# Optimization experiments

Measured on AMD Instinct MI355X. Metric: run time of the kernel, lower is better.

The kernel has to match this reference:

```python
import jax, jax.numpy as jnp
import numpy as np

WS = 32          # window_size -> N = WS*WS = 1024
DIM = 1024
HEADS = 16
BATCH = 16


def _local_mask():
    # token i maps to grid cell (i//WS, i%WS); attend iff within 3x3 neighborhood
    idx = jnp.arange(WS * WS)
    r, c = idx // WS, idx % WS
    return (jnp.abs(r[:, None] - r[None, :]) <= 1) & (jnp.abs(c[:, None] - c[None, :]) <= 1)


def setup_inputs() -> dict:
    key = jax.random.key(0)
    k1, k2, k3 = jax.random.split(key, 3)
    N = WS * WS
    x = jax.random.normal(k1, (BATCH, N, DIM), dtype=jnp.float32)
    w_qkv = jax.random.normal(k2, (3 * DIM, DIM), dtype=jnp.float32) * 0.02
    w_proj = jax.random.normal(k3, (DIM, DIM), dtype=jnp.float32) * 0.02
    b_proj = jnp.zeros((DIM,), dtype=jnp.float32)
    return {"x": x, "w_qkv": w_qkv, "w_proj": w_proj, "b_proj": b_proj}


def reference(x, w_qkv, w_proj, b_proj):
    B, N, C = x.shape
    H = HEADS
    D = C // H
    scale = D ** (-0.5)
    # qkv projection: torch Linear is x @ W^T
    qkv = (x @ w_qkv.T).reshape(B, N, 3, H, D).transpose(2, 0, 3, 1, 4)  # (3,B,H,N,D)
    q, k, v = qkv[0], qkv[1], qkv[2]
    attn = jnp.einsum('bhnd,bhmd->bhnm', q, k) * scale  # (B,H,N,N)
    mask = _local_mask()  # (N,N) bool
    attn = jnp.where(mask[None, None], attn, -jnp.inf)
    attn = jax.nn.softmax(attn, axis=-1)
    out = jnp.einsum('bhnm,bhmd->bhnd', attn, v)          # (B,H,N,D)
    out = out.transpose(0, 2, 1, 3).reshape(B, N, C)      # (B,N,C)
    return out @ w_proj.T + b_proj
```

## Files before the change

kernel.cpp:

```cpp
#include <hip/hip_runtime.h>
#include <hip/hip_bf16.h>
#include <stdint.h>


typedef __bf16 bf16;
typedef __bf16 bf16x4_t __attribute__((ext_vector_type(4)));
typedef __bf16 bf16x8_t __attribute__((ext_vector_type(8)));
typedef float f32x4_t __attribute__((ext_vector_type(4)));

static __device__ __forceinline__ void gload_lds16(const void* g, void* l) {
  __builtin_amdgcn_global_load_lds((__attribute__((address_space(1))) void*)g,
                                   (__attribute__((address_space(3))) void*)l,
                                   16, 0, 0);
}

static __device__ __forceinline__ void block_barrier() {
  asm volatile("" ::: "memory");
  __builtin_amdgcn_s_barrier();
  asm volatile("" ::: "memory");
}

__global__ void cvt_f32_bf16(const float* __restrict__ in, bf16* __restrict__ out, int n4) {
  int i = blockIdx.x * blockDim.x + threadIdx.x;
  if (i >= n4) return;
  float4 v = reinterpret_cast<const float4*>(in)[i];
  bf16x4_t o;
  o[0] = (bf16)v.x; o[1] = (bf16)v.y; o[2] = (bf16)v.z; o[3] = (bf16)v.w;
  reinterpret_cast<bf16x4_t*>(out)[i] = o;
}

template<int OUT_BF16>
__global__ __launch_bounds__(512, 2)
void gemm256(const bf16* __restrict__ A, const bf16* __restrict__ Bm,
             void* __restrict__ Cout, const float* __restrict__ bias,
             int M, int N, int K) {
  extern __shared__ __align__(16) bf16 lds[];

  const int tid = threadIdx.x;
  const int w = tid >> 6, lane = tid & 63;
  const int fr = lane & 15, g = lane >> 4;
  const int wr = w >> 2, wc = w & 3;

  const int nwg = gridDim.x * gridDim.y;
  int lid = blockIdx.y * gridDim.x + blockIdx.x;
  lid = (lid & 7) * (nwg >> 3) + (lid >> 3);
  const int bx = lid % gridDim.x, by = lid / gridDim.x;
  const int row0 = by * 256, col0 = bx * 256;

  const bf16* Ag = A + (size_t)row0 * K;
  const bf16* Bg = Bm + (size_t)col0 * K;
  const int rsub = tid >> 3;
  const int csw  = ((tid & 7) * 8) ^ ((rsub & 7) << 3);
  const int nkt  = K >> 6;

  f32x4_t acc[8][4] = {};

  auto stage = [&](int kt, int slot) {
    const int kb = kt << 6;
    bf16* sl = lds + slot * 32768;
#pragma unroll
    for (int n = 0; n < 4; ++n) {
      gload_lds16(Ag + (size_t)(rsub + n * 64) * K + kb + csw,
                  sl + n * 4096 + w * 512);
      gload_lds16(Bg + (size_t)(rsub + n * 64) * K + kb + csw,
                  sl + 16384 + n * 4096 + w * 512);
    }
  };

  const int axor = (fr & 7) << 4;

  stage(0, 0);
  stage(1, 1);
  asm volatile("s_waitcnt vmcnt(8)" ::: "memory");
  block_barrier();

  for (int kt = 0; kt < nkt; ++kt) {
    const char* cA = reinterpret_cast<const char*>(lds + (kt & 1) * 32768);
    const char* cB = cA + 32768;

    bf16x8_t a0[4][2], a1[4][2], b0[2][2], b1[2][2];

    auto lda = [&](bf16x8_t (&dst)[4][2], int q) {
#pragma unroll
      for (int i = 0; i < 4; ++i) {
        const int row = wr * 128 + (q * 4 + i) * 16 + fr;
#pragma unroll
        for (int kh = 0; kh < 2; ++kh) {
          const int bo = (row << 7) + (((kh << 6) + (g << 4)) ^ axor);
          dst[i][kh] = *reinterpret_cast<const bf16x8_t*>(cA + bo);
        }
      }
    };
    auto ldb = [&](bf16x8_t (&dst)[2][2], int q) {
#pragma unroll
      for (int j = 0; j < 2; ++j) {
        const int row = wc * 64 + (q * 2 + j) * 16 + fr;
#pragma unroll
        for (int kh = 0; kh < 2; ++kh) {
          const int bo = (row << 7) + (((kh << 6) + (g << 4)) ^ axor);
          dst[j][kh] = *reinterpret_cast<const bf16x8_t*>(cB + bo);
        }
      }
    };

    lda(a0, 0);
    ldb(b0, 0);
#pragma unroll
    for (int i = 0; i < 4; ++i)
#pragma unroll
      for (int j = 0; j < 2; ++j)
#pragma unroll
        for (int kh = 0; kh < 2; ++kh)
          acc[i][j] = __builtin_amdgcn_mfma_f32_16x16x32_bf16(
              a0[i][kh], b0[j][kh], acc[i][j], 0, 0, 0);
    ldb(b1, 1);
#pragma unroll
    for (int i = 0; i < 4; ++i)
#pragma unroll
      for (int j = 0; j < 2; ++j)
#pragma unroll
        for (int kh = 0; kh < 2; ++kh)
          acc[i][2 + j] = __builtin_amdgcn_mfma_f32_16x16x32_bf16(
              a0[i][kh], b1[j][kh], acc[i][2 + j], 0, 0, 0);
    lda(a1, 1);
#pragma unroll
    for (int i = 0; i < 4; ++i)
#pragma unroll
      for (int j = 0; j < 2; ++j)
#pragma unroll
        for (int kh = 0; kh < 2; ++kh)
          acc[4 + i][2 + j] = __builtin_amdgcn_mfma_f32_16x16x32_bf16(
              a1[i][kh], b1[j][kh], acc[4 + i][2 + j], 0, 0, 0);
#pragma unroll
    for (int i = 0; i < 4; ++i)
#pragma unroll
      for (int j = 0; j < 2; ++j)
#pragma unroll
        for (int kh = 0; kh < 2; ++kh)
          acc[4 + i][j] = __builtin_amdgcn_mfma_f32_16x16x32_bf16(
              a1[i][kh], b0[j][kh], acc[4 + i][j], 0, 0, 0);

    block_barrier();
    if (kt + 2 < nkt) stage(kt + 2, kt & 1);
    if (kt < nkt - 2) {
      asm volatile("s_waitcnt vmcnt(8)" ::: "memory");
    } else {
      asm volatile("s_waitcnt vmcnt(0)" ::: "memory");
    }
    block_barrier();
  }

#pragma unroll
  for (int fm = 0; fm < 8; ++fm) {
    const int rbase = row0 + wr * 128 + fm * 16 + g * 4;
#pragma unroll
    for (int fn = 0; fn < 4; ++fn) {
      const int col = col0 + wc * 64 + fn * 16 + fr;
#pragma unroll
      for (int r = 0; r < 4; ++r) {
        const size_t idx = (size_t)(rbase + r) * N + col;
        if constexpr (OUT_BF16) {
          reinterpret_cast<bf16*>(Cout)[idx] = (bf16)acc[fm][fn][r];
        } else {
          reinterpret_cast<float*>(Cout)[idx] = acc[fm][fn][r] + bias[col];
        }
      }
    }
  }
}

__global__ __launch_bounds__(256)
void local_attn(const bf16* __restrict__ qkv, bf16* __restrict__ outp) {
  const int tid  = threadIdx.x;
  const int wave = tid >> 6, lane = tid & 63;
  const int tsub = lane >> 3, ch = lane & 7;
  const int gt = (blockIdx.x * 4 + wave) * 8 + tsub;
  const int i  = gt & 1023;
  const int bh = gt >> 10;
  const int h  = bh & 15, b = bh >> 4;
  const int r  = i >> 5, c = i & 31;

  const bf16* base = qkv + (size_t)(b * 1024) * 3072 + h * 64 + ch * 8;

  bf16x8_t qv = *reinterpret_cast<const bf16x8_t*>(base + (size_t)i * 3072);
  float qf[8];
#pragma unroll
  for (int e = 0; e < 8; ++e) qf[e] = (float)qv[e];

  float s[9];
  bool valid[9];
#pragma unroll
  for (int dr = -1; dr <= 1; ++dr) {
#pragma unroll
    for (int dc = -1; dc <= 1; ++dc) {
      const int idx = (dr + 1) * 3 + (dc + 1);
      const int rr = r + dr, cc = c + dc;
      valid[idx] = (rr >= 0 && rr < 32 && cc >= 0 && cc < 32);
      float sv = -1e30f;
      if (valid[idx]) {
        const int j = rr * 32 + cc;
        bf16x8_t kv = *reinterpret_cast<const bf16x8_t*>(base + (size_t)j * 3072 + 1024);
        float ps = 0.f;
#pragma unroll
        for (int e = 0; e < 8; ++e) ps += qf[e] * (float)kv[e];
        ps += __shfl_xor(ps, 1);
        ps += __shfl_xor(ps, 2);
        ps += __shfl_xor(ps, 4);
        sv = ps * 0.125f;
      }
      s[idx] = sv;
    }
  }

  float mx = s[0];
#pragma unroll
  for (int t = 1; t < 9; ++t) mx = fmaxf(mx, s[t]);

  float p[9], denom = 0.f;
#pragma unroll
  for (int t = 0; t < 9; ++t) {
    p[t] = valid[t] ? __expf(s[t] - mx) : 0.f;
    denom += p[t];
  }

  float o[8] = {};
#pragma unroll
  for (int dr = -1; dr <= 1; ++dr) {
#pragma unroll
    for (int dc = -1; dc <= 1; ++dc) {
      const int idx = (dr + 1) * 3 + (dc + 1);
      if (valid[idx]) {
        const int j = (r + dr) * 32 + (c + dc);
        bf16x8_t vv = *reinterpret_cast<const bf16x8_t*>(base + (size_t)j * 3072 + 2048);
        const float pw = p[idx];
#pragma unroll
        for (int e = 0; e < 8; ++e) o[e] += pw * (float)vv[e];
      }
    }
  }

  const float inv = 1.f / denom;
  bf16x8_t ov;
#pragma unroll
  for (int e = 0; e < 8; ++e) ov[e] = (bf16)(o[e] * inv);
  *reinterpret_cast<bf16x8_t*>(outp + (size_t)(b * 1024 + i) * 1024 + h * 64 + ch * 8) = ov;
}

extern "C" void kernel_launch(void* const* d_in, const int* in_sizes, int n_in,
                              void* d_out, int out_size, void* d_ws, size_t ws_size,
                              hipStream_t stream) {
  const float* x      = (const float*)d_in[0];
  const float* w_qkv  = (const float*)d_in[1];
  const float* w_proj = (const float*)d_in[2];
  const float* b_proj = (const float*)d_in[3];
  float* out = (float*)d_out;

  const size_t nx   = (size_t)16384 * 1024;
  const size_t nwq  = (size_t)3072 * 1024;
  const size_t nwp  = (size_t)1024 * 1024;
  const size_t nqkv = (size_t)16384 * 3072;

  bf16* x_bf  = (bf16*)d_ws;
  bf16* wq_bf = x_bf + nx;
  bf16* wp_bf = wq_bf + nwq;
  bf16* qkv   = wp_bf + nwp;
  bf16* attn  = qkv + nqkv;

  (void)hipFuncSetAttribute((const void*)&gemm256<1>,
                            hipFuncAttributeMaxDynamicSharedMemorySize, 131072);
  (void)hipFuncSetAttribute((const void*)&gemm256<0>,
                            hipFuncAttributeMaxDynamicSharedMemorySize, 131072);

  cvt_f32_bf16<<<(int)(nx  / 4 / 256), 256, 0, stream>>>(x,      x_bf,  (int)(nx  / 4));
  cvt_f32_bf16<<<(int)(nwq / 4 / 256), 256, 0, stream>>>(w_qkv,  wq_bf, (int)(nwq / 4));
  cvt_f32_bf16<<<(int)(nwp / 4 / 256), 256, 0, stream>>>(w_proj, wp_bf, (int)(nwp / 4));

  gemm256<1><<<dim3(3072 / 256, 16384 / 256), 512, 131072, stream>>>(
      x_bf, wq_bf, qkv, nullptr, 16384, 3072, 1024);

  local_attn<<<8192, 256, 0, stream>>>(qkv, attn);

  gemm256<0><<<dim3(1024 / 256, 16384 / 256), 512, 131072, stream>>>(
      attn, wp_bf, out, b_proj, 16384, 1024, 1024);
}
```

Baseline: 216.1 us.

## Interleave GEMM prefetch with MFMA clusters and merge conversion kernels

The GEMM main loop is split into four MFMA clusters separated by block barriers and raised wave priority (s_setprio). The next tile's B and A global-to-LDS loads are now issued between clusters instead of after all compute, as soon as the corresponding LDS reads have drained. This aims to overlap memory traffic with matrix math and to coordinate the waves on each CU. The three fp32-to-bf16 conversion launches are also merged into one kernel to cut launch overhead. The extra barriers per iteration add synchronisation cost and could stall waves if the schedule does not line up.

```diff
diff --git a/kernel.cpp b/kernel.cpp
--- a/kernel.cpp
+++ b/kernel.cpp
@@ -20,13 +20,19 @@
   asm volatile("" ::: "memory");
 }
 
-__global__ void cvt_f32_bf16(const float* __restrict__ in, bf16* __restrict__ out, int n4) {
+__global__ void cvt_all(const float* __restrict__ x, const float* __restrict__ wq,
+                        const float* __restrict__ wp, bf16* __restrict__ xb,
+                        bf16* __restrict__ wqb, bf16* __restrict__ wpb) {
+  constexpr int NX = 4194304, NWQ = 786432;
   int i = blockIdx.x * blockDim.x + threadIdx.x;
-  if (i >= n4) return;
-  float4 v = reinterpret_cast<const float4*>(in)[i];
+  const float* src; bf16* dst; int off;
+  if (i < NX)            { src = x;  dst = xb;  off = i; }
+  else if (i < NX + NWQ) { src = wq; dst = wqb; off = i - NX; }
+  else                   { src = wp; dst = wpb; off = i - (NX + NWQ); }
+  float4 v = reinterpret_cast<const float4*>(src)[off];
   bf16x4_t o;
   o[0] = (bf16)v.x; o[1] = (bf16)v.y; o[2] = (bf16)v.z; o[3] = (bf16)v.w;
-  reinterpret_cast<bf16x4_t*>(out)[i] = o;
+  reinterpret_cast<bf16x4_t*>(dst)[off] = o;
 }
 
 template<int OUT_BF16>
@@ -55,28 +61,34 @@
 
   f32x4_t acc[8][4] = {};
 
-  auto stage = [&](int kt, int slot) {
+  auto stageA = [&](int kt, int slot) {
     const int kb = kt << 6;
     bf16* sl = lds + slot * 32768;
 #pragma unroll
-    for (int n = 0; n < 4; ++n) {
+    for (int n = 0; n < 4; ++n)
       gload_lds16(Ag + (size_t)(rsub + n * 64) * K + kb + csw,
                   sl + n * 4096 + w * 512);
+  };
+  auto stageB = [&](int kt, int slot) {
+    const int kb = kt << 6;
+    bf16* sl = lds + slot * 32768 + 16384;
+#pragma unroll
+    for (int n = 0; n < 4; ++n)
       gload_lds16(Bg + (size_t)(rsub + n * 64) * K + kb + csw,
-                  sl + 16384 + n * 4096 + w * 512);
-    }
+                  sl + n * 4096 + w * 512);
   };
 
   const int axor = (fr & 7) << 4;
 
-  stage(0, 0);
-  stage(1, 1);
+  stageB(0, 0); stageA(0, 0);
+  stageB(1, 1); stageA(1, 1);
   asm volatile("s_waitcnt vmcnt(8)" ::: "memory");
   block_barrier();
 
   for (int kt = 0; kt < nkt; ++kt) {
     const char* cA = reinterpret_cast<const char*>(lds + (kt & 1) * 32768);
     const char* cB = cA + 32768;
+    const bool pf = (kt + 2 < nkt);
 
     bf16x8_t a0[4][2], a1[4][2], b0[2][2], b1[2][2];
 
@@ -102,47 +114,47 @@
         }
       }
     };
-
-    lda(a0, 0);
-    ldb(b0, 0);
-#pragma unroll
-    for (int i = 0; i < 4; ++i)
-#pragma unroll
-      for (int j = 0; j < 2; ++j)
-#pragma unroll
-        for (int kh = 0; kh < 2; ++kh)
-          acc[i][j] = __builtin_amdgcn_mfma_f32_16x16x32_bf16(
-              a0[i][kh], b0[j][kh], acc[i][j], 0, 0, 0);
+    auto mfma16 = [&](bf16x8_t (&af)[4][2], bf16x8_t (&bf_)[2][2], int mi0, int nj0) {
+      __builtin_amdgcn_s_setprio(1);
+#pragma unroll
+      for (int i = 0; i < 4; ++i)
+#pragma unroll
+        for (int j = 0; j < 2; ++j)
+#pragma unroll
+          for (int kh = 0; kh < 2; ++kh)
+            acc[mi0 + i][nj0 + j] = __builtin_amdgcn_mfma_f32_16x16x32_bf16(
+                af[i][kh], bf_[j][kh], acc[mi0 + i][nj0 + j], 0, 0, 0);
+      __builtin_amdgcn_s_setprio(0);
+    };
+
+    lda(a0, 0); ldb(b0, 0);
+    asm volatile("s_waitcnt lgkmcnt(8)" ::: "memory");
+    block_barrier();
+    asm volatile("s_waitcnt lgkmcnt(0)" ::: "memory");
+    __builtin_amdgcn_sched_barrier(0);
+    mfma16(a0, b0, 0, 0);
+    block_barrier();
+
     ldb(b1, 1);
-#pragma unroll
-    for (int i = 0; i < 4; ++i)
-#pragma unroll
-      for (int j = 0; j < 2; ++j)
-#pragma unroll
-        for (int kh = 0; kh < 2; ++kh)
-          acc[i][2 + j] = __builtin_amdgcn_mfma_f32_16x16x32_bf16(
-              a0[i][kh], b1[j][kh], acc[i][2 + j], 0, 0, 0);
+    block_barrier();
+    asm volatile("s_waitcnt lgkmcnt(0)" ::: "memory");
+    __builtin_amdgcn_sched_barrier(0);
+    mfma16(a0, b1, 0, 2);
+    block_barrier();
+
     lda(a1, 1);
-#pragma unroll
-    for (int i = 0; i < 4; ++i)
-#pragma unroll
-      for (int j = 0; j < 2; ++j)
-#pragma unroll
-        for (int kh = 0; kh < 2; ++kh)
-          acc[4 + i][2 + j] = __builtin_amdgcn_mfma_f32_16x16x32_bf16(
-              a1[i][kh], b1[j][kh], acc[4 + i][2 + j], 0, 0, 0);
-#pragma unroll
-    for (int i = 0; i < 4; ++i)
-#pragma unroll
-      for (int j = 0; j < 2; ++j)
-#pragma unroll
-        for (int kh = 0; kh < 2; ++kh)
-          acc[4 + i][j] = __builtin_amdgcn_mfma_f32_16x16x32_bf16(
-              a1[i][kh], b0[j][kh], acc[4 + i][j], 0, 0, 0);
-
-    block_barrier();
-    if (kt + 2 < nkt) stage(kt + 2, kt & 1);
-    if (kt < nkt - 2) {
+    if (pf) stageB(kt + 2, kt & 1);
+    block_barrier();
+    asm volatile("s_waitcnt lgkmcnt(0)" ::: "memory");
+    __builtin_amdgcn_sched_barrier(0);
+    mfma16(a1, b1, 4, 2);
+    block_barrier();
+
+    if (pf) stageA(kt + 2, kt & 1);
+    block_barrier();
+    __builtin_amdgcn_sched_barrier(0);
+    mfma16(a1, b0, 4, 0);
+    if (pf) {
       asm volatile("s_waitcnt vmcnt(8)" ::: "memory");
     } else {
       asm volatile("s_waitcnt vmcnt(0)" ::: "memory");
@@ -271,9 +283,7 @@
   (void)hipFuncSetAttribute((const void*)&gemm256<0>,
                             hipFuncAttributeMaxDynamicSharedMemorySize, 131072);
 
-  cvt_f32_bf16<<<(int)(nx  / 4 / 256), 256, 0, stream>>>(x,      x_bf,  (int)(nx  / 4));
-  cvt_f32_bf16<<<(int)(nwq / 4 / 256), 256, 0, stream>>>(w_qkv,  wq_bf, (int)(nwq / 4));
-  cvt_f32_bf16<<<(int)(nwp / 4 / 256), 256, 0, stream>>>(w_proj, wp_bf, (int)(nwp / 4));
+  cvt_all<<<20480, 256, 0, stream>>>(x, w_qkv, w_proj, x_bf, wq_bf, wp_bf);
 
   gemm256<1><<<dim3(3072 / 256, 16384 / 256), 512, 131072, stream>>>(
       x_bf, wq_bf, qkv, nullptr, 16384, 3072, 1024);
```

After: 217.8 us. No clear change (+0.8%).

## Use BK=32 GEMM tiles, smaller proj M-tile, and fuse conversion kernels

Applied to the files above, without the earlier changes.

The GEMM k-tile shrinks from 64 to 32, which cuts LDS use per block from 128KB to 64KB or 48KB and changes the LDS swizzle to match. The output projection now uses 128-row tiles so it launches twice as many workgroups. The three f32->bf16 conversion launches are merged into one kernel. The smaller k-tile doubles the number of barriers and iterations and lowers the MFMA work done per sync, in return for lighter LDS pressure and better occupancy and grid fill.

```diff
diff --git a/kernel.cpp b/kernel.cpp
--- a/kernel.cpp
+++ b/kernel.cpp
@@ -20,21 +20,32 @@
   asm volatile("" ::: "memory");
 }
 
-__global__ void cvt_f32_bf16(const float* __restrict__ in, bf16* __restrict__ out, int n4) {
+__global__ void cvt_all(const float* __restrict__ x, const float* __restrict__ wq,
+                        const float* __restrict__ wp, bf16* __restrict__ xb,
+                        bf16* __restrict__ wqb, bf16* __restrict__ wpb) {
+  constexpr int NX = 4194304, NWQ = 786432;
   int i = blockIdx.x * blockDim.x + threadIdx.x;
-  if (i >= n4) return;
-  float4 v = reinterpret_cast<const float4*>(in)[i];
+  const float* src; bf16* dst; int off;
+  if (i < NX)            { src = x;  dst = xb;  off = i; }
+  else if (i < NX + NWQ) { src = wq; dst = wqb; off = i - NX; }
+  else                   { src = wp; dst = wpb; off = i - (NX + NWQ); }
+  float4 v = reinterpret_cast<const float4*>(src)[off];
   bf16x4_t o;
   o[0] = (bf16)v.x; o[1] = (bf16)v.y; o[2] = (bf16)v.z; o[3] = (bf16)v.w;
-  reinterpret_cast<bf16x4_t*>(out)[i] = o;
-}
-
-template<int OUT_BF16>
+  reinterpret_cast<bf16x4_t*>(dst)[off] = o;
+}
+
+template<int OUT_BF16, int MWF>
 __global__ __launch_bounds__(512, 2)
-void gemm256(const bf16* __restrict__ A, const bf16* __restrict__ Bm,
-             void* __restrict__ Cout, const float* __restrict__ bias,
-             int M, int N, int K) {
-  extern __shared__ __align__(16) bf16 lds[];
+void gemm_bk32(const bf16* __restrict__ A, const bf16* __restrict__ Bm,
+               void* __restrict__ Cout, const float* __restrict__ bias,
+               int M, int N, int K) {
+  constexpr int BM      = MWF * 32;
+  constexpr int A_BYTES = BM * 64;
+  constexpr int SLOT    = A_BYTES + 16384;
+  constexpr int ALOADS  = MWF / 4;
+  constexpr int LPT     = ALOADS + 2;
+  extern __shared__ __align__(16) char lds[];
 
   const int tid = threadIdx.x;
   const int w = tid >> 6, lane = tid & 63;
@@ -45,105 +56,91 @@
   int lid = blockIdx.y * gridDim.x + blockIdx.x;
   lid = (lid & 7) * (nwg >> 3) + (lid >> 3);
   const int bx = lid % gridDim.x, by = lid / gridDim.x;
-  const int row0 = by * 256, col0 = bx * 256;
+  const int row0 = by * BM, col0 = bx * 256;
 
   const bf16* Ag = A + (size_t)row0 * K;
   const bf16* Bg = Bm + (size_t)col0 * K;
-  const int rsub = tid >> 3;
-  const int csw  = ((tid & 7) * 8) ^ ((rsub & 7) << 3);
-  const int nkt  = K >> 6;
-
-  f32x4_t acc[8][4] = {};
+  const int srow = tid >> 2;
+  const int scol = ((tid & 3) ^ ((tid >> 3) & 3)) * 8;
+  const int nkt  = K >> 5;
+
+  f32x4_t acc[MWF][4] = {};
 
   auto stage = [&](int kt, int slot) {
-    const int kb = kt << 6;
-    bf16* sl = lds + slot * 32768;
-#pragma unroll
-    for (int n = 0; n < 4; ++n) {
-      gload_lds16(Ag + (size_t)(rsub + n * 64) * K + kb + csw,
-                  sl + n * 4096 + w * 512);
-      gload_lds16(Bg + (size_t)(rsub + n * 64) * K + kb + csw,
-                  sl + 16384 + n * 4096 + w * 512);
-    }
+    const int kb = kt << 5;
+    char* sb = lds + slot * SLOT;
+#pragma unroll
+    for (int n = 0; n < ALOADS; ++n)
+      gload_lds16(Ag + (size_t)(n * 128 + srow) * K + kb + scol,
+                  sb + n * 8192 + tid * 16);
+#pragma unroll
+    for (int n = 0; n < 2; ++n)
+      gload_lds16(Bg + (size_t)(n * 128 + srow) * K + kb + scol,
+                  sb + A_BYTES + n * 8192 + tid * 16);
   };
 
-  const int axor = (fr & 7) << 4;
+  const int uxor = ((fr >> 1) & 3) << 4;
 
   stage(0, 0);
   stage(1, 1);
-  asm volatile("s_waitcnt vmcnt(8)" ::: "memory");
+  if constexpr (LPT == 4) asm volatile("s_waitcnt vmcnt(4)" ::: "memory");
+  else                    asm volatile("s_waitcnt vmcnt(3)" ::: "memory");
   block_barrier();
 
   for (int kt = 0; kt < nkt; ++kt) {
-    const char* cA = reinterpret_cast<const char*>(lds + (kt & 1) * 32768);
-    const char* cB = cA + 32768;
-
-    bf16x8_t a0[4][2], a1[4][2], b0[2][2], b1[2][2];
-
-    auto lda = [&](bf16x8_t (&dst)[4][2], int q) {
-#pragma unroll
-      for (int i = 0; i < 4; ++i) {
-        const int row = wr * 128 + (q * 4 + i) * 16 + fr;
-#pragma unroll
-        for (int kh = 0; kh < 2; ++kh) {
-          const int bo = (row << 7) + (((kh << 6) + (g << 4)) ^ axor);
-          dst[i][kh] = *reinterpret_cast<const bf16x8_t*>(cA + bo);
-        }
+    const char* cA = lds + (kt & 1) * SLOT;
+    const char* cB = cA + A_BYTES;
+    const bool pf = (kt + 2 < nkt);
+
+    bf16x8_t a0[MWF / 2], a1[MWF / 2], b0[2], b1[2];
+
+    auto lda = [&](bf16x8_t (&dst)[MWF / 2], int q) {
+#pragma unroll
+      for (int i = 0; i < MWF / 2; ++i) {
+        const int row = wr * (MWF * 16) + (q * (MWF / 2) + i) * 16 + fr;
+        dst[i] = *reinterpret_cast<const bf16x8_t*>(cA + (row << 6) + ((g << 4) ^ uxor));
       }
     };
-    auto ldb = [&](bf16x8_t (&dst)[2][2], int q) {
+    auto ldb = [&](bf16x8_t (&dst)[2], int q) {
 #pragma unroll
       for (int j = 0; j < 2; ++j) {
         const int row = wc * 64 + (q * 2 + j) * 16 + fr;
-#pragma unroll
-        for (int kh = 0; kh < 2; ++kh) {
-          const int bo = (row << 7) + (((kh << 6) + (g << 4)) ^ axor);
-          dst[j][kh] = *reinterpret_cast<const bf16x8_t*>(cB + bo);
-        }
+        dst[j] = *reinterpret_cast<const bf16x8_t*>(cB + (row << 6) + ((g << 4) ^ uxor));
       }
     };
 
     lda(a0, 0);
     ldb(b0, 0);
 #pragma unroll
-    for (int i = 0; i < 4; ++i)
-#pragma unroll
-      for (int j = 0; j < 2; ++j)
-#pragma unroll
-        for (int kh = 0; kh < 2; ++kh)
-          acc[i][j] = __builtin_amdgcn_mfma_f32_16x16x32_bf16(
-              a0[i][kh], b0[j][kh], acc[i][j], 0, 0, 0);
+    for (int i = 0; i < MWF / 2; ++i)
+#pragma unroll
+      for (int j = 0; j < 2; ++j)
+        acc[i][j] = __builtin_amdgcn_mfma_f32_16x16x32_bf16(a0[i], b0[j], acc[i][j], 0, 0, 0);
     ldb(b1, 1);
 #pragma unroll
-    for (int i = 0; i < 4; ++i)
-#pragma unroll
-      for (int j = 0; j < 2; ++j)
-#pragma unroll
-        for (int kh = 0; kh < 2; ++kh)
-          acc[i][2 + j] = __builtin_amdgcn_mfma_f32_16x16x32_bf16(
-              a0[i][kh], b1[j][kh], acc[i][2 + j], 0, 0, 0);
+    for (int i = 0; i < MWF / 2; ++i)
+#pragma unroll
+      for (int j = 0; j < 2; ++j)
+        acc[i][2 + j] = __builtin_amdgcn_mfma_f32_16x16x32_bf16(a0[i], b1[j], acc[i][2 + j], 0, 0, 0);
     lda(a1, 1);
 #pragma unroll
-    for (int i = 0; i < 4; ++i)
-#pragma unroll
-      for (int j = 0; j < 2; ++j)
-#pragma unroll
-        for (int kh = 0; kh < 2; ++kh)
-          acc[4 + i][2 + j] = __builtin_amdgcn_mfma_f32_16x16x32_bf16(
-              a1[i][kh], b1[j][kh], acc[4 + i][2 + j], 0, 0, 0);
-#pragma unroll
-    for (int i = 0; i < 4; ++i)
-#pragma unroll
-      for (int j = 0; j < 2; ++j)
-#pragma unroll
-        for (int kh = 0; kh < 2; ++kh)
-          acc[4 + i][j] = __builtin_amdgcn_mfma_f32_16x16x32_bf16(
-              a1[i][kh], b0[j][kh], acc[4 + i][j], 0, 0, 0);
+    for (int i = 0; i < MWF / 2; ++i)
+#pragma unroll
+      for (int j = 0; j < 2; ++j)
+        acc[MWF / 2 + i][2 + j] = __builtin_amdgcn_mfma_f32_16x16x32_bf16(
+            a1[i], b1[j], acc[MWF / 2 + i][2 + j], 0, 0, 0);
+#pragma unroll
+    for (int i = 0; i < MWF / 2; ++i)
+#pragma unroll
+      for (int j = 0; j < 2; ++j)
+        acc[MWF / 2 + i][j] = __builtin_amdgcn_mfma_f32_16x16x32_bf16(
+            a1[i], b0[j], acc[MWF / 2 + i][j], 0, 0, 0);
 
     block_barrier();
-    if (kt + 2 < nkt) stage(kt + 2, kt & 1);
+    if (pf) stage(kt + 2, kt & 1);
     if (kt < nkt - 2) {
-      asm volatile("s_waitcnt vmcnt(8)" ::: "memory");
+      if constexpr (LPT == 4) asm volatile("s_waitcnt vmcnt(4)" ::: "memory");
+      else                    asm volatile("s_waitcnt vmcnt(3)" ::: "memory");
     } else {
       asm volatile("s_waitcnt vmcnt(0)" ::: "memory");
     }
@@ -151,8 +148,8 @@
   }
 
 #pragma unroll
-  for (int fm = 0; fm < 8; ++fm) {
-    const int rbase = row0 + wr * 128 + fm * 16 + g * 4;
+  for (int fm = 0; fm < MWF; ++fm) {
+    const int rbase = row0 + wr * (MWF * 16) + fm * 16 + g * 4;
 #pragma unroll
     for (int fn = 0; fn < 4; ++fn) {
       const int col = col0 + wc * 64 + fn * 16 + fr;
@@ -266,20 +263,18 @@
   bf16* qkv   = wp_bf + nwp;
   bf16* attn  = qkv + nqkv;
 
-  (void)hipFuncSetAttribute((const void*)&gemm256<1>,
-                            hipFuncAttributeMaxDynamicSharedMemorySize, 131072);
-  (void)hipFuncSetAttribute((const void*)&gemm256<0>,
-                            hipFuncAttributeMaxDynamicSharedMemorySize, 131072);
-
-  cvt_f32_bf16<<<(int)(nx  / 4 / 256), 256, 0, stream>>>(x,      x_bf,  (int)(nx  / 4));
-  cvt_f32_bf16<<<(int)(nwq / 4 / 256), 256, 0, stream>>>(w_qkv,  wq_bf, (int)(nwq / 4));
-  cvt_f32_bf16<<<(int)(nwp / 4 / 256), 256, 0, stream>>>(w_proj, wp_bf, (int)(nwp / 4));
-
-  gemm256<1><<<dim3(3072 / 256, 16384 / 256), 512, 131072, stream>>>(
+  (void)hipFuncSetAttribute((const void*)&gemm_bk32<1, 8>,
+                            hipFuncAttributeMaxDynamicSharedMemorySize, 65536);
+  (void)hipFuncSetAttribute((const void*)&gemm_bk32<0, 4>,
+                            hipFuncAttributeMaxDynamicSharedMemorySize, 49152);
+
+  cvt_all<<<20480, 256, 0, stream>>>(x, w_qkv, w_proj, x_bf, wq_bf, wp_bf);
+
+  gemm_bk32<1, 8><<<dim3(3072 / 256, 16384 / 256), 512, 65536, stream>>>(
       x_bf, wq_bf, qkv, nullptr, 16384, 3072, 1024);
 
   local_attn<<<8192, 256, 0, stream>>>(qkv, attn);
 
-  gemm256<0><<<dim3(1024 / 256, 16384 / 256), 512, 131072, stream>>>(
+  gemm_bk32<0, 4><<<dim3(1024 / 256, 16384 / 128), 512, 49152, stream>>>(
       attn, wp_bf, out, b_proj, 16384, 1024, 1024);
 }
```

After: 220.5 us. No clear change (+2.0%).
